# Kernel optimization log

Measured on AMD Instinct MI355X. Metric: run time of the kernel, lower is better.

## Reference

```python
import jax, jax.numpy as jnp
import numpy as np

B, T, D, H = 8, 2048, 1024, 128

def setup_inputs() -> dict:
    key = jax.random.key(0)
    ks = jax.random.split(key, 8)
    s = 1.0 / np.sqrt(D)
    return {
        "x": jax.random.normal(ks[0], (B, T, D), dtype=jnp.float32),
        "att": jax.random.normal(ks[1], (B, T, D), dtype=jnp.float32),
        "Wk": jax.random.uniform(ks[2], (D, H), minval=-s, maxval=s, dtype=jnp.float32),
        "bk": jax.random.uniform(ks[3], (H,), minval=-s, maxval=s, dtype=jnp.float32),
        "Wq": jax.random.uniform(ks[4], (D, H), minval=-s, maxval=s, dtype=jnp.float32),
        "bq": jax.random.uniform(ks[5], (H,), minval=-s, maxval=s, dtype=jnp.float32),
        "Wv": jax.random.uniform(ks[6], (D, H), minval=-s, maxval=s, dtype=jnp.float32),
        "bv": jax.random.uniform(ks[7], (H,), minval=-s, maxval=s, dtype=jnp.float32),
    }

def reference(x, att, Wk, bk, Wq, bq, Wv, bv):
    # k, q from `att`; v from `x` (as in the original module)
    k = jnp.einsum('btd,dh->bth', att, Wk) + bk   # [B,T,H]
    q = jnp.einsum('btd,dh->bth', att, Wq) + bq   # [B,T,H]
    v = jnp.einsum('btd,dh->bth', x, Wv) + bv     # [B,T,H]
    # Faithful to source: scores / head_size**(-0.5) == scores * sqrt(head_size)
    scale = jnp.asarray(k.shape[-1], jnp.float32) ** 0.5
    scores = jnp.einsum('bqh,bkh->bqk', q, k) * scale  # [B,T,T]
    att_mat = jax.nn.softmax(scores, axis=-1)
    # dropout p=0.0 -> identity (eval semantics)
    return jnp.einsum('bqk,bkh->bqh', att_mat, v)      # [B,T,H]
```

## Files before the change

kernel.cpp:

```cpp
#include <hip/hip_runtime.h>
#include <stdint.h>

typedef unsigned short u16;
typedef __attribute__((ext_vector_type(8))) short bf16x8;
typedef __attribute__((ext_vector_type(4))) float f32x4;
typedef __attribute__((ext_vector_type(16))) float f32x16;
typedef __attribute__((ext_vector_type(4))) uint32_t u32x4;
typedef __attribute__((ext_vector_type(2))) int int2v;

#define T_LEN 2048
#define D_DIM 1024
#define H_DIM 128
#define SCALE_LOG2 16.32223116f

#define EXP2F(x) __builtin_amdgcn_exp2f(x)

__device__ __forceinline__ u16 f2bf(float f) {
  uint32_t u = __float_as_uint(f);
  u += 0x7FFFu + ((u >> 16) & 1u);
  return (u16)(u >> 16);
}
__device__ __forceinline__ float bf2f(u16 h) { return __uint_as_float(((uint32_t)h) << 16); }

__device__ __forceinline__ void gload16(const void* g, void* l) {
  __builtin_amdgcn_global_load_lds(
      (const __attribute__((address_space(1))) uint32_t*)(uintptr_t)g,
      (__attribute__((address_space(3))) uint32_t*)(uint32_t)(uintptr_t)l,
      16, 0, 0);
}

#define VMCNT0() asm volatile("s_waitcnt vmcnt(0)" ::: "memory")
#define VMLG0() asm volatile("s_waitcnt vmcnt(0) lgkmcnt(0)" ::: "memory")
#define VM2LG0() asm volatile("s_waitcnt vmcnt(2) lgkmcnt(0)" ::: "memory")
#define BAR() __builtin_amdgcn_s_barrier()
#define PRIO(n) __builtin_amdgcn_s_setprio(n)

#define MFMA(a, b, c) __builtin_amdgcn_mfma_f32_16x16x32_bf16((a), (b), (c), 0, 0, 0)
#define MFMA32(a, b, c) __builtin_amdgcn_mfma_f32_32x32x16_bf16((a), (b), (c), 0, 0, 0)

__device__ __forceinline__ uint32_t cvtpk(float lo, float hi) {
  uint32_t r;
  asm("v_cvt_pk_bf16_f32 %0, %1, %2" : "=v"(r) : "v"(lo), "v"(hi));
  return r;
}
__device__ __forceinline__ void plswap(uint32_t& a, uint32_t& b, int hi) {
#if __has_builtin(__builtin_amdgcn_permlane32_swap)
  int2v r = __builtin_amdgcn_permlane32_swap((int)a, (int)b, false, false);
  a = (uint32_t)r.x;
  b = (uint32_t)r.y;
#else
  uint32_t as = (uint32_t)__shfl_xor((int)a, 32);
  uint32_t bs = (uint32_t)__shfl_xor((int)b, 32);
  uint32_t na = hi ? bs : a;
  uint32_t nb = hi ? b : as;
  a = na;
  b = nb;
#endif
}

__global__ __launch_bounds__(256) void prep_w(
    const float* __restrict__ Wk, const float* __restrict__ Wq, const float* __restrict__ Wv,
    u16* __restrict__ wqh, u16* __restrict__ wql,
    u16* __restrict__ wkh, u16* __restrict__ wkl,
    u16* __restrict__ wvh) {
  __shared__ u16 th[3][128][16];
  __shared__ u16 tl[2][128][16];
  const int i = threadIdx.x;
  const int d0 = blockIdx.x * 16;
  const int dl = i >> 4;
  const int hb = (i & 15) * 8;
  const int d = d0 + dl;
#pragma unroll
  for (int e = 0; e < 8; ++e) {
    int h = hb + e;
    float q = Wq[d * H_DIM + h] * SCALE_LOG2;
    float k = Wk[d * H_DIM + h];
    float v = Wv[d * H_DIM + h];
    u16 qh = f2bf(q); th[0][h][dl] = qh; tl[0][h][dl] = f2bf(q - bf2f(qh));
    u16 kh = f2bf(k); th[1][h][dl] = kh; tl[1][h][dl] = f2bf(k - bf2f(kh));
    th[2][h][dl] = f2bf(v);
  }
  __syncthreads();
  const int h = i >> 1, c = i & 1;
  u16* planes[5] = {wqh, wql, wkh, wkl, wvh};
  const u16* srcs[5] = {&th[0][0][0], &tl[0][0][0], &th[1][0][0], &tl[1][0][0], &th[2][0][0]};
#pragma unroll
  for (int p = 0; p < 5; ++p) {
    bf16x8 v8 = *(const bf16x8*)(srcs[p] + h * 16 + c * 8);
    *(bf16x8*)(planes[p] + h * 1024 + d0 + c * 8) = v8;
  }
}

#define QBUF 53248

__global__ __launch_bounds__(512) void qkv_proj(
    const float* __restrict__ att, const float* __restrict__ x,
    const u16* __restrict__ wqh, const u16* __restrict__ wql,
    const u16* __restrict__ wkh, const u16* __restrict__ wkl,
    const u16* __restrict__ wvh,
    const float* __restrict__ bq, const float* __restrict__ bk, const float* __restrict__ bv,
    u16* __restrict__ qhp, u16* __restrict__ qlp,
    u16* __restrict__ khp, u16* __restrict__ klp,
    u16* __restrict__ vtp) {
  __shared__ __attribute__((aligned(128))) char lds[104 * 1024];

  const int tid = threadIdx.x;
  const int wid = tid >> 6;
  const int ln = tid & 63;
  const int g = ln >> 4;
  const int cl = ln & 15;
  const int t0g = blockIdx.x * 64;

  const f32x4 fz = {0.f, 0.f, 0.f, 0.f};
  f32x4 accq[4], acck[4], accv[4];
#pragma unroll
  for (int s = 0; s < 4; ++s) { accq[s] = fz; acck[s] = fz; accv[s] = fz; }

  const int isA = tid < 256;
  const int at = tid & 255;
  const int arow = at >> 2;
  const int ac = at & 3;
  const float* srcp = (isA ? att : x) + (size_t)(t0g + arow) * D_DIM + ac * 8;
  const int aw_off = (isA ? 0 : 8192) + arow * 64 + ((ac ^ ((arow >> 1) & 3)) * 16);

  auto STAGE_W = [&](int b, int ks) {
    char* wt = lds + b * QBUF + 12288;
#pragma unroll
    for (int j = 0; j < 5; ++j) {
      int seg = wid * 5 + j;
      int p = seg >> 3;
      int s = seg & 7;
      int db = s * 1024 + ln * 16;
      int row = db >> 6;
      int c = (db >> 4) & 3;
      int cs = c ^ ((row >> 1) & 3);
      const u16* wp = (p == 0) ? wqh : (p == 1) ? wql : (p == 2) ? wkh : (p == 3) ? wkl : wvh;
      gload16(wp + row * 1024 + ks * 32 + cs * 8, wt + p * 8192 + s * 1024);
    }
  };
  auto CWRITE_A = [&](int b, f32x4 f0, f32x4 f1) {
    bf16x8 vh, vl;
#pragma unroll
    for (int e = 0; e < 4; ++e) {
      u16 h0 = f2bf(f0[e]); vh[e] = (short)h0; vl[e] = (short)f2bf(f0[e] - bf2f(h0));
      u16 h1 = f2bf(f1[e]); vh[e + 4] = (short)h1; vl[e + 4] = (short)f2bf(f1[e] - bf2f(h1));
    }
    char* dst = lds + b * QBUF + aw_off;
    *(bf16x8*)dst = vh;
    if (isA) *(bf16x8*)(dst + 4096) = vl;
  };

  {
    f32x4 f0 = *(const f32x4*)(srcp);
    f32x4 f1 = *(const f32x4*)(srcp + 4);
    STAGE_W(0, 0);
    CWRITE_A(0, f0, f1);
  }
  f32x4 pA0 = *(const f32x4*)(srcp + 32);
  f32x4 pA1 = *(const f32x4*)(srcp + 36);
  VMLG0();
  BAR();

  int cur = 0;
  for (int ks = 0; ks < 32; ++ks) {
    if (ks < 31) STAGE_W(cur ^ 1, ks + 1);
    f32x4 nA0, nA1;
    if (ks < 30) {
      nA0 = *(const f32x4*)(srcp + (ks + 2) * 32);
      nA1 = *(const f32x4*)(srcp + (ks + 2) * 32 + 4);
    }
    char* base = lds + cur * QBUF;
    char* wt = base + 12288;
    bf16x8 ah[4], al[4], xh[4];
#pragma unroll
    for (int s = 0; s < 4; ++s) {
      int row = s * 16 + cl;
      int byte = row * 64 + ((g ^ ((row >> 1) & 3)) * 16);
      ah[s] = *(const bf16x8*)(base + byte);
      al[s] = *(const bf16x8*)(base + 4096 + byte);
      xh[s] = *(const bf16x8*)(base + 8192 + byte);
    }
    {
      int hrow = wid * 16 + cl;
      int wb = hrow * 64 + ((g ^ ((hrow >> 1) & 3)) * 16);
      bf16x8 bqh_ = *(const bf16x8*)(wt + 0 * 8192 + wb);
      bf16x8 bql_ = *(const bf16x8*)(wt + 1 * 8192 + wb);
      bf16x8 bkh_ = *(const bf16x8*)(wt + 2 * 8192 + wb);
      bf16x8 bkl_ = *(const bf16x8*)(wt + 3 * 8192 + wb);
      bf16x8 bvh_ = *(const bf16x8*)(wt + 4 * 8192 + wb);
      PRIO(1);
#pragma unroll
      for (int s = 0; s < 4; ++s) {
        accq[s] = MFMA(ah[s], bqh_, accq[s]);
        accq[s] = MFMA(al[s], bqh_, accq[s]);
        accq[s] = MFMA(ah[s], bql_, accq[s]);
        acck[s] = MFMA(ah[s], bkh_, acck[s]);
        acck[s] = MFMA(al[s], bkh_, acck[s]);
        acck[s] = MFMA(ah[s], bkl_, acck[s]);
        accv[s] = MFMA(xh[s], bvh_, accv[s]);
      }
      PRIO(0);
    }
    if (ks < 31) CWRITE_A(cur ^ 1, pA0, pA1);
    pA0 = nA0;
    pA1 = nA1;
    if (ks < 30) VM2LG0(); else VMLG0();
    BAR();
    cur ^= 1;
  }

  char* vbuf = lds;
  {
    int h = wid * 16 + cl;
    float bqv = bq[h] * SCALE_LOG2, bkv = bk[h], bvv = bv[h];
#pragma unroll
    for (int s = 0; s < 4; ++s) {
#pragma unroll
      for (int r = 0; r < 4; ++r) {
        int t = s * 16 + g * 4 + r;
        size_t idx = (size_t)(t0g + t) * H_DIM + h;
        float qv = accq[s][r] + bqv;
        u16 qh_ = f2bf(qv);
        qhp[idx] = qh_;
        qlp[idx] = f2bf(qv - bf2f(qh_));
        float kv = acck[s][r] + bkv;
        u16 kh_ = f2bf(kv);
        khp[idx] = kh_;
        klp[idx] = f2bf(kv - bf2f(kh_));
        float vv = accv[s][r] + bvv;
        int c3 = t >> 3;
        int byte = h * 128 + ((c3 ^ (h & 7)) * 16) + (t & 7) * 2;
        *(u16*)(vbuf + byte) = f2bf(vv);
      }
    }
  }
  __syncthreads();
  {
    int h = tid >> 2, qtr = tid & 3;
    int b2 = t0g >> 11;
    int tb = t0g & 2047;
    u16* dst = vtp + ((size_t)(b2 * H_DIM + h)) * T_LEN + tb + qtr * 16;
#pragma unroll
    for (int c2 = 0; c2 < 2; ++c2) {
      int c3 = qtr * 2 + c2;
      bf16x8 v8 = *(const bf16x8*)(vbuf + h * 128 + ((c3 ^ (h & 7)) * 16));
      *(bf16x8*)(dst + c2 * 8) = v8;
    }
  }
}

#define KVB 32
#define NT 16

__global__ __launch_bounds__(512, 2) void attn(
    const u16* __restrict__ qhp, const u16* __restrict__ qlp,
    const u16* __restrict__ khp, const u16* __restrict__ klp,
    const u16* __restrict__ vtp,
    float* __restrict__ out) {
  __shared__ __attribute__((aligned(128))) char lds[128 * 1024];

  const int tid = threadIdx.x;
  const int w = tid >> 6;
  const int l = tid & 63;
  const int q5 = l & 31;
  const int hi = l >> 5;
  const int wq = w >> 2;
  const int kvq = w & 3;
  const int pi = wq;
  const int bid = blockIdx.x;
  const int b_ = bid & 7;
  const int t0 = (bid >> 3) * 64;
  const int qrow = t0 + wq * 32 + q5;
  const int kv0q = kvq * 512;

  bf16x8 qh[8], ql[8];
  {
    const u16* qb = qhp + (size_t)(b_ * T_LEN + qrow) * H_DIM + hi * 8;
    const u16* qlb = qlp + (size_t)(b_ * T_LEN + qrow) * H_DIM + hi * 8;
#pragma unroll
    for (int kc = 0; kc < 8; ++kc) {
      qh[kc] = *(const bf16x8*)(qb + kc * 16);
      ql[kc] = *(const bf16x8*)(qlb + kc * 16);
    }
  }

  uint32_t sgoff[8];
#pragma unroll
  for (int i = 0; i < 8; ++i) {
    int gid = i * 128 + pi * 64 + l;
    int plane = gid >> 9;
    int n = gid & 511;
    int row = n >> 4;
    int slot = n & 15;
    int dg = slot ^ (row & 15);
    sgoff[i] = (uint32_t)(plane * 2097152 + (b_ * T_LEN + row) * H_DIM + dg * 8);
  }
  char* const qbuf0 = lds + kvq * 2 * 16384;

  auto STAGE = [&](int b, int kvoff) {
    char* buf = qbuf0 + b * 16384;
#pragma unroll
    for (int i = 0; i < 8; ++i)
      gload16(khp + sgoff[i] + (uint32_t)(kvoff * H_DIM), buf + i * 2048 + pi * 1024);
  };

  f32x16 o[4] = {};
  float m_ = -1e30f;
  float l_ = 0.f;
  f32x16 s_prev;

  auto SMPV = [&](const bf16x8* vfr) {
    float t01 = fmaxf(s_prev[0], s_prev[1]), t23 = fmaxf(s_prev[2], s_prev[3]);
    float t45 = fmaxf(s_prev[4], s_prev[5]), t67 = fmaxf(s_prev[6], s_prev[7]);
    float t89 = fmaxf(s_prev[8], s_prev[9]), tab = fmaxf(s_prev[10], s_prev[11]);
    float tcd = fmaxf(s_prev[12], s_prev[13]), tef = fmaxf(s_prev[14], s_prev[15]);
    float q0 = fmaxf(t01, t23), q1 = fmaxf(t45, t67);
    float q2 = fmaxf(t89, tab), q3 = fmaxf(tcd, tef);
    float pmax = fmaxf(fmaxf(q0, q1), fmaxf(q2, q3));
    pmax = fmaxf(pmax, __shfl_xor(pmax, 32));
    if (__any(pmax > m_ + 8.f)) {
      float mn = fmaxf(m_, pmax);
      float sf = EXP2F(m_ - mn);
      m_ = mn;
      l_ *= sf;
#pragma unroll
      for (int j = 0; j < 16; ++j) {
        int rj = (j & 3) + 8 * (j >> 2) + 4 * hi;
        float sfj = __shfl(sf, rj);
        o[0][j] *= sfj; o[1][j] *= sfj; o[2][j] *= sfj; o[3][j] *= sfj;
      }
    }
    float p[16];
#pragma unroll
    for (int j = 0; j < 16; ++j) p[j] = EXP2F(s_prev[j] - m_);
    float a0 = p[0] + p[1], a1 = p[2] + p[3], a2 = p[4] + p[5], a3 = p[6] + p[7];
    float a4 = p[8] + p[9], a5 = p[10] + p[11], a6 = p[12] + p[13], a7 = p[14] + p[15];
    float b0 = a0 + a1, b1 = a2 + a3, b2 = a4 + a5, b3 = a6 + a7;
    float ps = (b0 + b1) + (b2 + b3);
    ps += __shfl_xor(ps, 32);
    l_ += ps;

    uint32_t u0 = cvtpk(p[0], p[1]), v0 = cvtpk(p[4], p[5]);
    uint32_t u1 = cvtpk(p[2], p[3]), v1 = cvtpk(p[6], p[7]);
    uint32_t u2 = cvtpk(p[8], p[9]), v2 = cvtpk(p[12], p[13]);
    uint32_t u3 = cvtpk(p[10], p[11]), v3 = cvtpk(p[14], p[15]);
    plswap(u0, v0, hi);
    plswap(u1, v1, hi);
    plswap(u2, v2, hi);
    plswap(u3, v3, hi);
    u32x4 f0w = {u0, u1, v0, v1};
    u32x4 f1w = {u2, u3, v2, v3};
    bf16x8 pa0 = *(bf16x8*)&f0w;
    bf16x8 pa1 = *(bf16x8*)&f1w;
#pragma unroll
    for (int nt = 0; nt < 4; ++nt) o[nt] = MFMA32(pa0, vfr[nt], o[nt]);
#pragma unroll
    for (int nt = 0; nt < 4; ++nt) o[nt] = MFMA32(pa1, vfr[4 + nt], o[nt]);
  };

  auto LOADV = [&](int tv, bf16x8* vfr) {
#pragma unroll
    for (int ks = 0; ks < 2; ++ks)
#pragma unroll
      for (int nt = 0; nt < 4; ++nt)
        vfr[ks * 4 + nt] = *(const bf16x8*)(
            vtp + (size_t)(b_ * H_DIM + nt * 32 + q5) * T_LEN +
            kv0q + tv * KVB + ks * 16 + hi * 8);
  };

  STAGE(0, kv0q);
  VMCNT0();
  BAR();

  for (int t = 0; t < NT; ++t) {
    if (t + 1 < NT) STAGE((t + 1) & 1, kv0q + (t + 1) * KVB);
    bf16x8 vfr[8];
    if (t > 0) LOADV(t - 1, vfr);

    const char* kb = qbuf0 + (t & 1) * 16384 + q5 * 256;
    f32x16 s0 = {}, s1 = {}, s2 = {};
    PRIO(1);
#pragma unroll
    for (int kc = 0; kc < 8; ++kc) {
      int slot = (((kc * 2 + hi) ^ (q5 & 15)) * 16);
      bf16x8 kh_f = *(const bf16x8*)(kb + slot);
      bf16x8 kl_f = *(const bf16x8*)(kb + 8192 + slot);
      s0 = MFMA32(kh_f, qh[kc], s0);
      s1 = MFMA32(kl_f, qh[kc], s1);
      s2 = MFMA32(kh_f, ql[kc], s2);
    }
    PRIO(0);

    if (t > 0) SMPV(vfr);

    s_prev = (s0 + s1) + s2;
    if (t == 0) VMCNT0();
    BAR();
  }

  {
    bf16x8 vfr[8];
    LOADV(NT - 1, vfr);
    SMPV(vfr);
  }

  float* mlb = (float*)(lds + 96 * 1024);
  __syncthreads();
  if (hi == 0) {
    mlb[(wq * 4 + kvq) * 64 + q5 * 2] = m_;
    mlb[(wq * 4 + kvq) * 64 + q5 * 2 + 1] = l_;
  }
  __syncthreads();
  float sc;
  {
    float ms0 = mlb[(wq * 4 + 0) * 64 + q5 * 2], ls0 = mlb[(wq * 4 + 0) * 64 + q5 * 2 + 1];
    float ms1 = mlb[(wq * 4 + 1) * 64 + q5 * 2], ls1 = mlb[(wq * 4 + 1) * 64 + q5 * 2 + 1];
    float ms2 = mlb[(wq * 4 + 2) * 64 + q5 * 2], ls2 = mlb[(wq * 4 + 2) * 64 + q5 * 2 + 1];
    float ms3 = mlb[(wq * 4 + 3) * 64 + q5 * 2], ls3 = mlb[(wq * 4 + 3) * 64 + q5 * 2 + 1];
    float mM = fmaxf(fmaxf(ms0, ms1), fmaxf(ms2, ms3));
    float L = ls0 * EXP2F(ms0 - mM) + ls1 * EXP2F(ms1 - mM) +
              ls2 * EXP2F(ms2 - mM) + ls3 * EXP2F(ms3 - mM);
    sc = EXP2F(m_ - mM) / L;
  }
#pragma unroll
  for (int j = 0; j < 16; ++j) {
    int rj = (j & 3) + 8 * (j >> 2) + 4 * hi;
    float scj = __shfl(sc, rj);
    o[0][j] *= scj; o[1][j] *= scj; o[2][j] *= scj; o[3][j] *= scj;
  }
  if (kvq != 0) {
    float* ob = (float*)(lds + (wq * 3 + (kvq - 1)) * 16384);
#pragma unroll
    for (int nt = 0; nt < 4; ++nt)
#pragma unroll
      for (int j = 0; j < 16; ++j) ob[nt * 1024 + j * 64 + l] = o[nt][j];
  }
  __syncthreads();
  if (kvq == 0) {
    float* ob0 = (float*)(lds + (wq * 3 + 0) * 16384);
    float* ob1 = (float*)(lds + (wq * 3 + 1) * 16384);
    float* ob2 = (float*)(lds + (wq * 3 + 2) * 16384);
#pragma unroll
    for (int j = 0; j < 16; ++j) {
      int rj = (j & 3) + 8 * (j >> 2) + 4 * hi;
      size_t rbase = (size_t)(b_ * T_LEN + t0 + wq * 32 + rj) * H_DIM + q5;
#pragma unroll
      for (int nt = 0; nt < 4; ++nt) {
        int oi = nt * 1024 + j * 64 + l;
        out[rbase + nt * 32] = o[nt][j] + ob0[oi] + ob1[oi] + ob2[oi];
      }
    }
  }
}

extern "C" void kernel_launch(void* const* d_in, const int* in_sizes, int n_in,
                              void* d_out, int out_size, void* d_ws, size_t ws_size,
                              hipStream_t stream) {
  const float* x   = (const float*)d_in[0];
  const float* att = (const float*)d_in[1];
  const float* Wk  = (const float*)d_in[2];
  const float* bk  = (const float*)d_in[3];
  const float* Wq  = (const float*)d_in[4];
  const float* bq  = (const float*)d_in[5];
  const float* Wv  = (const float*)d_in[6];
  const float* bv  = (const float*)d_in[7];
  float* out = (float*)d_out;
  char* ws = (char*)d_ws;

  u16* wqh = (u16*)(ws);
  u16* wql = (u16*)(ws + 256 * 1024);
  u16* wkh = (u16*)(ws + 512 * 1024);
  u16* wkl = (u16*)(ws + 768 * 1024);
  u16* wvh = (u16*)(ws + 1024 * 1024);
  u16* qhp = (u16*)(ws + (size_t)2 * 1024 * 1024);
  u16* qlp = (u16*)(ws + (size_t)6 * 1024 * 1024);
  u16* khp = (u16*)(ws + (size_t)10 * 1024 * 1024);
  u16* klp = (u16*)(ws + (size_t)14 * 1024 * 1024);
  u16* vtp = (u16*)(ws + (size_t)18 * 1024 * 1024);

  prep_w<<<64, 256, 0, stream>>>(Wk, Wq, Wv, wqh, wql, wkh, wkl, wvh);
  qkv_proj<<<256, 512, 0, stream>>>(att, x, wqh, wql, wkh, wkl, wvh,
                                    bq, bk, bv, qhp, qlp, khp, klp, vtp);
  attn<<<256, 512, 0, stream>>>(qhp, qlp, khp, klp, vtp, out);
}
```

Before: 274.9 us.

## Halve block size and tile height in projection and attention kernels, restructure pipelines

Both qkv_proj and attn now use 256-thread blocks covering 32 rows instead of 512 threads covering 64, and launch twice as many blocks. The aim is more blocks per CU with a smaller LDS footprint. qkv_proj drops its LDS double buffering for a single-buffer loop with a barrier before and after each k-step. attn drops its double-buffered K staging and per-iteration barriers: each wave stages its own K slice and waits on vmcnt, with V register prefetch overlapped with softmax and PV. The cost is fewer MFMAs per LDS load in the projection and less latency hiding there, since loads are exposed behind the full wait.

```diff
diff --git a/kernel.cpp b/kernel.cpp
--- a/kernel.cpp
+++ b/kernel.cpp
@@ -2,6 +2,7 @@
 #include <stdint.h>
 
 typedef unsigned short u16;
+typedef __attribute__((ext_vector_type(4))) short short4v;
 typedef __attribute__((ext_vector_type(8))) short bf16x8;
 typedef __attribute__((ext_vector_type(4))) float f32x4;
 typedef __attribute__((ext_vector_type(16))) float f32x16;
@@ -29,9 +30,9 @@
       16, 0, 0);
 }
 
-#define VMCNT0() asm volatile("s_waitcnt vmcnt(0)" ::: "memory")
 #define VMLG0() asm volatile("s_waitcnt vmcnt(0) lgkmcnt(0)" ::: "memory")
-#define VM2LG0() asm volatile("s_waitcnt vmcnt(2) lgkmcnt(0)" ::: "memory")
+#define VMC8() asm volatile("s_waitcnt vmcnt(8)" ::: "memory")
+#define CFENCE() asm volatile("" ::: "memory")
 #define BAR() __builtin_amdgcn_s_barrier()
 #define PRIO(n) __builtin_amdgcn_s_setprio(n)
 
@@ -91,9 +92,7 @@
   }
 }
 
-#define QBUF 53248
-
-__global__ __launch_bounds__(512) void qkv_proj(
+__global__ __launch_bounds__(256) void qkv_proj(
     const float* __restrict__ att, const float* __restrict__ x,
     const u16* __restrict__ wqh, const u16* __restrict__ wql,
     const u16* __restrict__ wkh, const u16* __restrict__ wkl,
@@ -102,32 +101,33 @@
     u16* __restrict__ qhp, u16* __restrict__ qlp,
     u16* __restrict__ khp, u16* __restrict__ klp,
     u16* __restrict__ vtp) {
-  __shared__ __attribute__((aligned(128))) char lds[104 * 1024];
+  __shared__ __attribute__((aligned(128))) char lds[46 * 1024];
+  char* const wt = lds + 6144;
 
   const int tid = threadIdx.x;
   const int wid = tid >> 6;
   const int ln = tid & 63;
   const int g = ln >> 4;
   const int cl = ln & 15;
-  const int t0g = blockIdx.x * 64;
+  const int t0g = blockIdx.x * 32;
 
   const f32x4 fz = {0.f, 0.f, 0.f, 0.f};
-  f32x4 accq[4], acck[4], accv[4];
-#pragma unroll
-  for (int s = 0; s < 4; ++s) { accq[s] = fz; acck[s] = fz; accv[s] = fz; }
-
-  const int isA = tid < 256;
-  const int at = tid & 255;
-  const int arow = at >> 2;
-  const int ac = at & 3;
-  const float* srcp = (isA ? att : x) + (size_t)(t0g + arow) * D_DIM + ac * 8;
-  const int aw_off = (isA ? 0 : 8192) + arow * 64 + ((ac ^ ((arow >> 1) & 3)) * 16);
-
-  auto STAGE_W = [&](int b, int ks) {
-    char* wt = lds + b * QBUF + 12288;
-#pragma unroll
-    for (int j = 0; j < 5; ++j) {
-      int seg = wid * 5 + j;
+  f32x4 accq[2][2], acck[2][2], accv[2][2];
+#pragma unroll
+  for (int a = 0; a < 2; ++a)
+#pragma unroll
+    for (int s = 0; s < 2; ++s) { accq[a][s] = fz; acck[a][s] = fz; accv[a][s] = fz; }
+
+  const int arow = tid >> 3;
+  const int ac = tid & 7;
+  const float* srcA = att + (size_t)(t0g + arow) * D_DIM + ac * 4;
+  const float* srcX = x + (size_t)(t0g + arow) * D_DIM + ac * 4;
+  const int awb = arow * 64 + (((ac >> 1) ^ ((arow >> 1) & 3)) * 16) + (ac & 1) * 8;
+
+  auto STAGE_W = [&](int ks) {
+#pragma unroll
+    for (int j = 0; j < 10; ++j) {
+      int seg = wid * 10 + j;
       int p = seg >> 3;
       int s = seg & 7;
       int db = s * 1024 + ln * 16;
@@ -138,112 +138,120 @@
       gload16(wp + row * 1024 + ks * 32 + cs * 8, wt + p * 8192 + s * 1024);
     }
   };
-  auto CWRITE_A = [&](int b, f32x4 f0, f32x4 f1) {
-    bf16x8 vh, vl;
+  auto CWRITE_A = [&](f32x4 fa, f32x4 fx) {
+    short4v vh, vl, vx;
 #pragma unroll
     for (int e = 0; e < 4; ++e) {
-      u16 h0 = f2bf(f0[e]); vh[e] = (short)h0; vl[e] = (short)f2bf(f0[e] - bf2f(h0));
-      u16 h1 = f2bf(f1[e]); vh[e + 4] = (short)h1; vl[e + 4] = (short)f2bf(f1[e] - bf2f(h1));
-    }
-    char* dst = lds + b * QBUF + aw_off;
-    *(bf16x8*)dst = vh;
-    if (isA) *(bf16x8*)(dst + 4096) = vl;
-  };
-
-  {
-    f32x4 f0 = *(const f32x4*)(srcp);
-    f32x4 f1 = *(const f32x4*)(srcp + 4);
-    STAGE_W(0, 0);
-    CWRITE_A(0, f0, f1);
-  }
-  f32x4 pA0 = *(const f32x4*)(srcp + 32);
-  f32x4 pA1 = *(const f32x4*)(srcp + 36);
-  VMLG0();
-  BAR();
-
-  int cur = 0;
+      u16 h0 = f2bf(fa[e]); vh[e] = (short)h0; vl[e] = (short)f2bf(fa[e] - bf2f(h0));
+      vx[e] = (short)f2bf(fx[e]);
+    }
+    *(short4v*)(lds + awb) = vh;
+    *(short4v*)(lds + 2048 + awb) = vl;
+    *(short4v*)(lds + 4096 + awb) = vx;
+  };
+
+  f32x4 pA = *(const f32x4*)(srcA);
+  f32x4 pX = *(const f32x4*)(srcX);
+
   for (int ks = 0; ks < 32; ++ks) {
-    if (ks < 31) STAGE_W(cur ^ 1, ks + 1);
-    f32x4 nA0, nA1;
-    if (ks < 30) {
-      nA0 = *(const f32x4*)(srcp + (ks + 2) * 32);
-      nA1 = *(const f32x4*)(srcp + (ks + 2) * 32 + 4);
-    }
-    char* base = lds + cur * QBUF;
-    char* wt = base + 12288;
-    bf16x8 ah[4], al[4], xh[4];
-#pragma unroll
-    for (int s = 0; s < 4; ++s) {
+    if (ks) BAR();
+    CWRITE_A(pA, pX);
+    STAGE_W(ks);
+    VMLG0();
+    BAR();
+    if (ks < 31) {
+      pA = *(const f32x4*)(srcA + (ks + 1) * 32);
+      pX = *(const f32x4*)(srcX + (ks + 1) * 32);
+    }
+    bf16x8 ah[2], al[2], xh[2];
+#pragma unroll
+    for (int s = 0; s < 2; ++s) {
       int row = s * 16 + cl;
       int byte = row * 64 + ((g ^ ((row >> 1) & 3)) * 16);
-      ah[s] = *(const bf16x8*)(base + byte);
-      al[s] = *(const bf16x8*)(base + 4096 + byte);
-      xh[s] = *(const bf16x8*)(base + 8192 + byte);
-    }
-    {
-      int hrow = wid * 16 + cl;
+      ah[s] = *(const bf16x8*)(lds + byte);
+      al[s] = *(const bf16x8*)(lds + 2048 + byte);
+      xh[s] = *(const bf16x8*)(lds + 4096 + byte);
+    }
+    bf16x8 bqh_[2], bql_[2], bkh_[2], bkl_[2], bvh_[2];
+#pragma unroll
+    for (int lnt = 0; lnt < 2; ++lnt) {
+      int hrow = (2 * wid + lnt) * 16 + cl;
       int wb = hrow * 64 + ((g ^ ((hrow >> 1) & 3)) * 16);
-      bf16x8 bqh_ = *(const bf16x8*)(wt + 0 * 8192 + wb);
-      bf16x8 bql_ = *(const bf16x8*)(wt + 1 * 8192 + wb);
-      bf16x8 bkh_ = *(const bf16x8*)(wt + 2 * 8192 + wb);
-      bf16x8 bkl_ = *(const bf16x8*)(wt + 3 * 8192 + wb);
-      bf16x8 bvh_ = *(const bf16x8*)(wt + 4 * 8192 + wb);
-      PRIO(1);
-#pragma unroll
-      for (int s = 0; s < 4; ++s) {
-        accq[s] = MFMA(ah[s], bqh_, accq[s]);
-        accq[s] = MFMA(al[s], bqh_, accq[s]);
-        accq[s] = MFMA(ah[s], bql_, accq[s]);
-        acck[s] = MFMA(ah[s], bkh_, acck[s]);
-        acck[s] = MFMA(al[s], bkh_, acck[s]);
-        acck[s] = MFMA(ah[s], bkl_, acck[s]);
-        accv[s] = MFMA(xh[s], bvh_, accv[s]);
-      }
-      PRIO(0);
-    }
-    if (ks < 31) CWRITE_A(cur ^ 1, pA0, pA1);
-    pA0 = nA0;
-    pA1 = nA1;
-    if (ks < 30) VM2LG0(); else VMLG0();
-    BAR();
-    cur ^= 1;
-  }
-
+      bqh_[lnt] = *(const bf16x8*)(wt + 0 * 8192 + wb);
+      bql_[lnt] = *(const bf16x8*)(wt + 1 * 8192 + wb);
+      bkh_[lnt] = *(const bf16x8*)(wt + 2 * 8192 + wb);
+      bkl_[lnt] = *(const bf16x8*)(wt + 3 * 8192 + wb);
+      bvh_[lnt] = *(const bf16x8*)(wt + 4 * 8192 + wb);
+    }
+    PRIO(1);
+#pragma unroll
+    for (int lnt = 0; lnt < 2; ++lnt)
+#pragma unroll
+      for (int s = 0; s < 2; ++s) accq[lnt][s] = MFMA(ah[s], bqh_[lnt], accq[lnt][s]);
+#pragma unroll
+    for (int lnt = 0; lnt < 2; ++lnt)
+#pragma unroll
+      for (int s = 0; s < 2; ++s) accq[lnt][s] = MFMA(al[s], bqh_[lnt], accq[lnt][s]);
+#pragma unroll
+    for (int lnt = 0; lnt < 2; ++lnt)
+#pragma unroll
+      for (int s = 0; s < 2; ++s) accq[lnt][s] = MFMA(ah[s], bql_[lnt], accq[lnt][s]);
+#pragma unroll
+    for (int lnt = 0; lnt < 2; ++lnt)
+#pragma unroll
+      for (int s = 0; s < 2; ++s) acck[lnt][s] = MFMA(ah[s], bkh_[lnt], acck[lnt][s]);
+#pragma unroll
+    for (int lnt = 0; lnt < 2; ++lnt)
+#pragma unroll
+      for (int s = 0; s < 2; ++s) acck[lnt][s] = MFMA(al[s], bkh_[lnt], acck[lnt][s]);
+#pragma unroll
+    for (int lnt = 0; lnt < 2; ++lnt)
+#pragma unroll
+      for (int s = 0; s < 2; ++s) acck[lnt][s] = MFMA(ah[s], bkl_[lnt], acck[lnt][s]);
+#pragma unroll
+    for (int lnt = 0; lnt < 2; ++lnt)
+#pragma unroll
+      for (int s = 0; s < 2; ++s) accv[lnt][s] = MFMA(xh[s], bvh_[lnt], accv[lnt][s]);
+    PRIO(0);
+  }
+
+  __syncthreads();
   char* vbuf = lds;
-  {
-    int h = wid * 16 + cl;
+#pragma unroll
+  for (int lnt = 0; lnt < 2; ++lnt) {
+    int h = (2 * wid + lnt) * 16 + cl;
     float bqv = bq[h] * SCALE_LOG2, bkv = bk[h], bvv = bv[h];
 #pragma unroll
-    for (int s = 0; s < 4; ++s) {
+    for (int s = 0; s < 2; ++s) {
 #pragma unroll
       for (int r = 0; r < 4; ++r) {
         int t = s * 16 + g * 4 + r;
         size_t idx = (size_t)(t0g + t) * H_DIM + h;
-        float qv = accq[s][r] + bqv;
+        float qv = accq[lnt][s][r] + bqv;
         u16 qh_ = f2bf(qv);
         qhp[idx] = qh_;
         qlp[idx] = f2bf(qv - bf2f(qh_));
-        float kv = acck[s][r] + bkv;
+        float kv = acck[lnt][s][r] + bkv;
         u16 kh_ = f2bf(kv);
         khp[idx] = kh_;
         klp[idx] = f2bf(kv - bf2f(kh_));
-        float vv = accv[s][r] + bvv;
+        float vv = accv[lnt][s][r] + bvv;
         int c3 = t >> 3;
-        int byte = h * 128 + ((c3 ^ (h & 7)) * 16) + (t & 7) * 2;
+        int byte = h * 64 + ((c3 ^ (h & 3)) * 16) + (t & 7) * 2;
         *(u16*)(vbuf + byte) = f2bf(vv);
       }
     }
   }
   __syncthreads();
   {
-    int h = tid >> 2, qtr = tid & 3;
+    int h = tid >> 1, half = tid & 1;
     int b2 = t0g >> 11;
     int tb = t0g & 2047;
-    u16* dst = vtp + ((size_t)(b2 * H_DIM + h)) * T_LEN + tb + qtr * 16;
+    u16* dst = vtp + ((size_t)(b2 * H_DIM + h)) * T_LEN + tb + half * 16;
 #pragma unroll
     for (int c2 = 0; c2 < 2; ++c2) {
-      int c3 = qtr * 2 + c2;
-      bf16x8 v8 = *(const bf16x8*)(vbuf + h * 128 + ((c3 ^ (h & 7)) * 16));
+      int c3 = half * 2 + c2;
+      bf16x8 v8 = *(const bf16x8*)(vbuf + h * 64 + ((c3 ^ (h & 3)) * 16));
       *(bf16x8*)(dst + c2 * 8) = v8;
     }
   }
@@ -252,25 +260,22 @@
 #define KVB 32
 #define NT 16
 
-__global__ __launch_bounds__(512, 2) void attn(
+__global__ __launch_bounds__(256, 2) void attn(
     const u16* __restrict__ qhp, const u16* __restrict__ qlp,
     const u16* __restrict__ khp, const u16* __restrict__ klp,
     const u16* __restrict__ vtp,
     float* __restrict__ out) {
-  __shared__ __attribute__((aligned(128))) char lds[128 * 1024];
+  __shared__ __attribute__((aligned(128))) char lds[64 * 1024];
 
   const int tid = threadIdx.x;
-  const int w = tid >> 6;
+  const int kvq = tid >> 6;
   const int l = tid & 63;
   const int q5 = l & 31;
   const int hi = l >> 5;
-  const int wq = w >> 2;
-  const int kvq = w & 3;
-  const int pi = wq;
   const int bid = blockIdx.x;
   const int b_ = bid & 7;
-  const int t0 = (bid >> 3) * 64;
-  const int qrow = t0 + wq * 32 + q5;
+  const int t0 = (bid >> 3) * 32;
+  const int qrow = t0 + q5;
   const int kv0q = kvq * 512;
 
   bf16x8 qh[8], ql[8];
@@ -284,32 +289,58 @@
     }
   }
 
-  uint32_t sgoff[8];
-#pragma unroll
-  for (int i = 0; i < 8; ++i) {
-    int gid = i * 128 + pi * 64 + l;
-    int plane = gid >> 9;
-    int n = gid & 511;
-    int row = n >> 4;
-    int slot = n & 15;
+  uint32_t sgoff[16];
+#pragma unroll
+  for (int i = 0; i < 16; ++i) {
+    int n = i * 64 + l;
+    int plane = n >> 9;
+    int m = n & 511;
+    int row = m >> 4;
+    int slot = m & 15;
     int dg = slot ^ (row & 15);
     sgoff[i] = (uint32_t)(plane * 2097152 + (b_ * T_LEN + row) * H_DIM + dg * 8);
   }
-  char* const qbuf0 = lds + kvq * 2 * 16384;
-
-  auto STAGE = [&](int b, int kvoff) {
-    char* buf = qbuf0 + b * 16384;
-#pragma unroll
-    for (int i = 0; i < 8; ++i)
-      gload16(khp + sgoff[i] + (uint32_t)(kvoff * H_DIM), buf + i * 2048 + pi * 1024);
+  char* const kbase = lds + kvq * 16384;
+
+  auto STAGE = [&](int kvoff) {
+#pragma unroll
+    for (int i = 0; i < 16; ++i)
+      gload16(khp + sgoff[i] + (uint32_t)(kvoff * H_DIM), kbase + i * 1024);
+  };
+  auto LOADV = [&](int tv, bf16x8* v) {
+#pragma unroll
+    for (int ks = 0; ks < 2; ++ks)
+#pragma unroll
+      for (int nt = 0; nt < 4; ++nt)
+        v[ks * 4 + nt] = *(const bf16x8*)(
+            vtp + (size_t)(b_ * H_DIM + nt * 32 + q5) * T_LEN +
+            kv0q + tv * KVB + ks * 16 + hi * 8);
   };
 
   f32x16 o[4] = {};
   float m_ = -1e30f;
   float l_ = 0.f;
   f32x16 s_prev;
-
-  auto SMPV = [&](const bf16x8* vfr) {
+  bf16x8 vfr[8], vnx[8];
+
+  auto QKT = [&]() {
+    const char* kb = kbase + q5 * 256;
+    f32x16 s0 = {}, s1 = {}, s2 = {};
+    PRIO(1);
+#pragma unroll
+    for (int kc = 0; kc < 8; ++kc) {
+      int so = (((kc * 2 + hi) ^ (q5 & 15)) * 16);
+      bf16x8 khf = *(const bf16x8*)(kb + so);
+      bf16x8 klf = *(const bf16x8*)(kb + 8192 + so);
+      s0 = MFMA32(khf, qh[kc], s0);
+      s1 = MFMA32(klf, qh[kc], s1);
+      s2 = MFMA32(khf, ql[kc], s2);
+    }
+    PRIO(0);
+    s_prev = (s0 + s1) + s2;
+  };
+
+  auto SMPV = [&]() {
     float t01 = fmaxf(s_prev[0], s_prev[1]), t23 = fmaxf(s_prev[2], s_prev[3]);
     float t45 = fmaxf(s_prev[4], s_prev[5]), t67 = fmaxf(s_prev[6], s_prev[7]);
     float t89 = fmaxf(s_prev[8], s_prev[9]), tab = fmaxf(s_prev[10], s_prev[11]);
@@ -352,71 +383,47 @@
     u32x4 f1w = {u2, u3, v2, v3};
     bf16x8 pa0 = *(bf16x8*)&f0w;
     bf16x8 pa1 = *(bf16x8*)&f1w;
+    PRIO(1);
 #pragma unroll
     for (int nt = 0; nt < 4; ++nt) o[nt] = MFMA32(pa0, vfr[nt], o[nt]);
 #pragma unroll
     for (int nt = 0; nt < 4; ++nt) o[nt] = MFMA32(pa1, vfr[4 + nt], o[nt]);
-  };
-
-  auto LOADV = [&](int tv, bf16x8* vfr) {
-#pragma unroll
-    for (int ks = 0; ks < 2; ++ks)
-#pragma unroll
-      for (int nt = 0; nt < 4; ++nt)
-        vfr[ks * 4 + nt] = *(const bf16x8*)(
-            vtp + (size_t)(b_ * H_DIM + nt * 32 + q5) * T_LEN +
-            kv0q + tv * KVB + ks * 16 + hi * 8);
-  };
-
-  STAGE(0, kv0q);
-  VMCNT0();
-  BAR();
-
-  for (int t = 0; t < NT; ++t) {
-    if (t + 1 < NT) STAGE((t + 1) & 1, kv0q + (t + 1) * KVB);
-    bf16x8 vfr[8];
-    if (t > 0) LOADV(t - 1, vfr);
-
-    const char* kb = qbuf0 + (t & 1) * 16384 + q5 * 256;
-    f32x16 s0 = {}, s1 = {}, s2 = {};
-    PRIO(1);
-#pragma unroll
-    for (int kc = 0; kc < 8; ++kc) {
-      int slot = (((kc * 2 + hi) ^ (q5 & 15)) * 16);
-      bf16x8 kh_f = *(const bf16x8*)(kb + slot);
-      bf16x8 kl_f = *(const bf16x8*)(kb + 8192 + slot);
-      s0 = MFMA32(kh_f, qh[kc], s0);
-      s1 = MFMA32(kl_f, qh[kc], s1);
-      s2 = MFMA32(kh_f, ql[kc], s2);
-    }
     PRIO(0);
-
-    if (t > 0) SMPV(vfr);
-
-    s_prev = (s0 + s1) + s2;
-    if (t == 0) VMCNT0();
-    BAR();
-  }
-
-  {
-    bf16x8 vfr[8];
-    LOADV(NT - 1, vfr);
-    SMPV(vfr);
-  }
-
-  float* mlb = (float*)(lds + 96 * 1024);
+  };
+
+  STAGE(kv0q);
+  LOADV(0, vnx);
+  VMC8();
+  QKT();
+#pragma unroll
+  for (int nt = 0; nt < 8; ++nt) vfr[nt] = vnx[nt];
+  CFENCE();
+
+  for (int t = 1; t < NT; ++t) {
+    STAGE(kv0q + t * KVB);
+    LOADV(t, vnx);
+    SMPV();
+    VMC8();
+    QKT();
+#pragma unroll
+    for (int nt = 0; nt < 8; ++nt) vfr[nt] = vnx[nt];
+    CFENCE();
+  }
+  SMPV();
+
+  float* mlb = (float*)(lds + 63 * 1024);
   __syncthreads();
   if (hi == 0) {
-    mlb[(wq * 4 + kvq) * 64 + q5 * 2] = m_;
-    mlb[(wq * 4 + kvq) * 64 + q5 * 2 + 1] = l_;
+    mlb[kvq * 64 + q5 * 2] = m_;
+    mlb[kvq * 64 + q5 * 2 + 1] = l_;
   }
   __syncthreads();
   float sc;
   {
-    float ms0 = mlb[(wq * 4 + 0) * 64 + q5 * 2], ls0 = mlb[(wq * 4 + 0) * 64 + q5 * 2 + 1];
-    float ms1 = mlb[(wq * 4 + 1) * 64 + q5 * 2], ls1 = mlb[(wq * 4 + 1) * 64 + q5 * 2 + 1];
-    float ms2 = mlb[(wq * 4 + 2) * 64 + q5 * 2], ls2 = mlb[(wq * 4 + 2) * 64 + q5 * 2 + 1];
-    float ms3 = mlb[(wq * 4 + 3) * 64 + q5 * 2], ls3 = mlb[(wq * 4 + 3) * 64 + q5 * 2 + 1];
+    float ms0 = mlb[0 * 64 + q5 * 2], ls0 = mlb[0 * 64 + q5 * 2 + 1];
+    float ms1 = mlb[1 * 64 + q5 * 2], ls1 = mlb[1 * 64 + q5 * 2 + 1];
+    float ms2 = mlb[2 * 64 + q5 * 2], ls2 = mlb[2 * 64 + q5 * 2 + 1];
+    float ms3 = mlb[3 * 64 + q5 * 2], ls3 = mlb[3 * 64 + q5 * 2 + 1];
     float mM = fmaxf(fmaxf(ms0, ms1), fmaxf(ms2, ms3));
     float L = ls0 * EXP2F(ms0 - mM) + ls1 * EXP2F(ms1 - mM) +
               ls2 * EXP2F(ms2 - mM) + ls3 * EXP2F(ms3 - mM);
@@ -429,7 +436,7 @@
     o[0][j] *= scj; o[1][j] *= scj; o[2][j] *= scj; o[3][j] *= scj;
   }
   if (kvq != 0) {
-    float* ob = (float*)(lds + (wq * 3 + (kvq - 1)) * 16384);
+    float* ob = (float*)(lds + (kvq - 1) * 16384);
 #pragma unroll
     for (int nt = 0; nt < 4; ++nt)
 #pragma unroll
@@ -437,13 +444,13 @@
   }
   __syncthreads();
   if (kvq == 0) {
-    float* ob0 = (float*)(lds + (wq * 3 + 0) * 16384);
-    float* ob1 = (float*)(lds + (wq * 3 + 1) * 16384);
-    float* ob2 = (float*)(lds + (wq * 3 + 2) * 16384);
+    float* ob0 = (float*)(lds + 0 * 16384);
+    float* ob1 = (float*)(lds + 1 * 16384);
+    float* ob2 = (float*)(lds + 2 * 16384);
 #pragma unroll
     for (int j = 0; j < 16; ++j) {
       int rj = (j & 3) + 8 * (j >> 2) + 4 * hi;
-      size_t rbase = (size_t)(b_ * T_LEN + t0 + wq * 32 + rj) * H_DIM + q5;
+      size_t rbase = (size_t)(b_ * T_LEN + t0 + rj) * H_DIM + q5;
 #pragma unroll
       for (int nt = 0; nt < 4; ++nt) {
         int oi = nt * 1024 + j * 64 + l;
@@ -479,7 +486,7 @@
   u16* vtp = (u16*)(ws + (size_t)18 * 1024 * 1024);
 
   prep_w<<<64, 256, 0, stream>>>(Wk, Wq, Wv, wqh, wql, wkh, wkl, wvh);
-  qkv_proj<<<256, 512, 0, stream>>>(att, x, wqh, wql, wkh, wkl, wvh,
+  qkv_proj<<<512, 256, 0, stream>>>(att, x, wqh, wql, wkh, wkl, wvh,
                                     bq, bk, bv, qhp, qlp, khp, klp, vtp);
-  attn<<<256, 512, 0, stream>>>(qhp, qlp, khp, klp, vtp, out);
-}
+  attn<<<512, 256, 0, stream>>>(qhp, qlp, khp, klp, vtp, out);
+}
```

After: 292.1 us. +6.3%, slower.
